# Performance work log

Measured on AMD Instinct MI355X. Metric: run time of the kernel, lower is better.

Reference implementation:

```python
import jax, jax.numpy as jnp
import numpy as np

N, F, E, T = 50000, 128, 800000, 8


def setup_inputs() -> dict:
    key = jax.random.key(0)
    ks = jax.random.split(key, 10)
    s = 1.0 / np.sqrt(F)
    return {
        "x": jax.random.normal(ks[0], (N, F), jnp.float32),
        "edge_index": jax.random.randint(ks[1], (2, E), 0, N, jnp.int64),
        "edge_weight": jax.random.uniform(ks[2], (E,), jnp.float32),
        "W0": jax.random.normal(ks[3], (F, F), jnp.float32) * s,
        "Wih": jax.random.normal(ks[4], (3 * F, F), jnp.float32) * s,
        "Whh": jax.random.normal(ks[5], (3 * F, F), jnp.float32) * s,
        "bih": jax.random.normal(ks[6], (3 * F,), jnp.float32) * s,
        "bhh": jax.random.normal(ks[7], (3 * F,), jnp.float32) * s,
        "Wlin": jax.random.normal(ks[8], (T, F), jnp.float32) * s,
        "blin": jax.random.normal(ks[9], (T,), jnp.float32) * s,
    }


def _evolve_weight(W0, Wih, Whh, bih, bhh):
    # One GRU step with input = hidden = W0 (rows of weight matrix as batch).
    gi = W0 @ Wih.T + bih  # [F, 3F]
    gh = W0 @ Whh.T + bhh
    ir, iz, inn = jnp.split(gi, 3, axis=1)
    hr, hz, hn = jnp.split(gh, 3, axis=1)
    r = jax.nn.sigmoid(ir + hr)
    z = jax.nn.sigmoid(iz + hz)
    n = jnp.tanh(inn + r * hn)
    return (1.0 - z) * n + z * W0  # [F, F]


def reference(x, edge_index, edge_weight, W0, Wih, Whh, bih, bhh, Wlin, blin):
    n_nodes = x.shape[0]
    W = _evolve_weight(W0, Wih, Whh, bih, bhh)
    # gcn_norm with added self-loops (fill value 1.0), symmetric normalization
    loop = jnp.arange(n_nodes, dtype=edge_index.dtype)
    row = jnp.concatenate([edge_index[0], loop])
    col = jnp.concatenate([edge_index[1], loop])
    ew = jnp.concatenate([edge_weight, jnp.ones((n_nodes,), edge_weight.dtype)])
    deg = jax.ops.segment_sum(ew, col, num_segments=n_nodes)
    dinv = jnp.where(deg > 0, jax.lax.rsqrt(jnp.where(deg > 0, deg, 1.0)), 0.0)
    norm = dinv[row] * ew * dinv[col]  # [E+N]
    xw = x @ W  # [N, F]
    h = jax.ops.segment_sum(norm[:, None] * xw[row], col, num_segments=n_nodes)
    h = jax.nn.relu(h)
    return h @ Wlin.T + blin  # [N, n_target]
```

## Files before the change

### kernel.cpp

```cpp
#include <hip/hip_runtime.h>
#include <math.h>

#define F 128
#define FIX_SCALE 16777216.0f
#define FIX_INV   (1.0f / 16777216.0f)
#define CNT_SHIFT 40
#define DEG_MASK  ((1ULL << 40) - 1)
#define EVB 256

using bf16x8 = __attribute__((ext_vector_type(8))) short;
using f32x4  = __attribute__((ext_vector_type(4))) float;

__device__ inline int read_idx(const int* ei, long long elem, int i64) {
    return i64 ? (int)((const long long*)ei)[elem] : ei[elem];
}
__device__ inline unsigned int f2bf_rn(float f) {
    unsigned int b = __float_as_uint(f);
    return (b + 0x7FFFu + ((b >> 16) & 1u)) >> 16;
}
__device__ inline float bflo(unsigned int u) { return __uint_as_float(u << 16); }
__device__ inline float bfhi(unsigned int u) { return __uint_as_float(u & 0xFFFF0000u); }

__device__ inline void acc8(float* acc, float wt, uint4 v) {
    acc[0] += wt * bflo(v.x); acc[1] += wt * bfhi(v.x);
    acc[2] += wt * bflo(v.y); acc[3] += wt * bfhi(v.y);
    acc[4] += wt * bflo(v.z); acc[5] += wt * bfhi(v.z);
    acc[6] += wt * bflo(v.w); acc[7] += wt * bfhi(v.w);
}

__global__ void k_init(unsigned long long* packed8, int* flag, const int* ei, int M8) {
    int i = blockIdx.x * blockDim.x + threadIdx.x;
    if (i < M8) packed8[i] = 0ULL;
    if (i == 0) {
        int i64 = 1;
        for (int j = 0; j < 32; ++j) if (ei[2 * j + 1] != 0) { i64 = 0; break; }
        *flag = i64;
    }
}

__global__ __launch_bounds__(256) void k_count_evolve(
        const int* __restrict__ ei, const float* __restrict__ ew,
        unsigned long long* __restrict__ packed8, int* __restrict__ pos,
        const int* __restrict__ flag, int E, int N,
        const float* __restrict__ W0, const float* __restrict__ Wih,
        const float* __restrict__ Whh, const float* __restrict__ bih,
        const float* __restrict__ bhh,
        unsigned short* __restrict__ Wth, unsigned short* __restrict__ Wtl) {
    int wave = threadIdx.x >> 6, lane = threadIdx.x & 63;
    if ((int)blockIdx.x >= EVB) {
        int e = ((int)blockIdx.x - EVB) * 256 + threadIdx.x;
        if (e >= E) return;
        int i64 = *flag;
        int c = read_idx(ei, (long long)E + e, i64);
        int copy = blockIdx.x & 7;
        unsigned long long u = (1ULL << CNT_SHIFT) |
                               (unsigned long long)(ew[e] * FIX_SCALE + 0.5f);
        unsigned long long old = atomicAdd(&packed8[(size_t)copy * N + c], u);
        pos[e] = (int)(((unsigned int)(old >> CNT_SHIFT)) | ((unsigned int)copy << 24));
        return;
    }
    int gw = (int)blockIdx.x * 4 + wave;
    int pairBase = gw * 16;
    int i = pairBase >> 7;
    int jb = pairBase & 127;
    int lp = lane & 15, sl = lane >> 4;
    int j = jb + lp;
    const float* w0p = W0 + (size_t)i * F;
    const float* pir = Wih + (size_t)j * F;
    const float* piz = Wih + (size_t)(j + F) * F;
    const float* pin = Wih + (size_t)(j + 2 * F) * F;
    const float* phr = Whh + (size_t)j * F;
    const float* phz = Whh + (size_t)(j + F) * F;
    const float* phn = Whh + (size_t)(j + 2 * F) * F;
    float air = 0, aiz = 0, ain = 0, ahr = 0, ahz = 0, ahn = 0;
    int k0 = sl * 32;
    #pragma unroll
    for (int kk = 0; kk < 32; kk += 4) {
        int k = k0 + kk;
        float4 w0 = *(const float4*)&w0p[k];
        float4 a;
        a = *(const float4*)&pir[k]; air += w0.x*a.x + w0.y*a.y + w0.z*a.z + w0.w*a.w;
        a = *(const float4*)&piz[k]; aiz += w0.x*a.x + w0.y*a.y + w0.z*a.z + w0.w*a.w;
        a = *(const float4*)&pin[k]; ain += w0.x*a.x + w0.y*a.y + w0.z*a.z + w0.w*a.w;
        a = *(const float4*)&phr[k]; ahr += w0.x*a.x + w0.y*a.y + w0.z*a.z + w0.w*a.w;
        a = *(const float4*)&phz[k]; ahz += w0.x*a.x + w0.y*a.y + w0.z*a.z + w0.w*a.w;
        a = *(const float4*)&phn[k]; ahn += w0.x*a.x + w0.y*a.y + w0.z*a.z + w0.w*a.w;
    }
    air += __shfl_xor(air, 16, 64); air += __shfl_xor(air, 32, 64);
    aiz += __shfl_xor(aiz, 16, 64); aiz += __shfl_xor(aiz, 32, 64);
    ain += __shfl_xor(ain, 16, 64); ain += __shfl_xor(ain, 32, 64);
    ahr += __shfl_xor(ahr, 16, 64); ahr += __shfl_xor(ahr, 32, 64);
    ahz += __shfl_xor(ahz, 16, 64); ahz += __shfl_xor(ahz, 32, 64);
    ahn += __shfl_xor(ahn, 16, 64); ahn += __shfl_xor(ahn, 32, 64);
    if (sl == 0) {
        air += bih[j];          ahr += bhh[j];
        aiz += bih[j + F];      ahz += bhh[j + F];
        ain += bih[j + 2 * F];  ahn += bhh[j + 2 * F];
        float r = 1.0f / (1.0f + expf(-(air + ahr)));
        float z = 1.0f / (1.0f + expf(-(aiz + ahz)));
        float n = tanhf(ain + r * ahn);
        float w = (1.0f - z) * n + z * w0p[j];
        unsigned int hb = f2bf_rn(w);
        float whi = __uint_as_float(hb << 16);
        unsigned int lb = f2bf_rn(w - whi);
        Wth[j * F + i] = (unsigned short)hb;
        Wtl[j * F + i] = (unsigned short)lb;
    }
}

__global__ void k_bsum(const unsigned long long* __restrict__ packed8,
                       int* __restrict__ bsum, int N) {
    __shared__ int s[4];
    int i = blockIdx.x * 256 + threadIdx.x;
    int v = 0;
    if (i < N) {
        #pragma unroll
        for (int k = 0; k < 8; ++k)
            v += (int)(packed8[(size_t)k * N + i] >> CNT_SHIFT);
    }
    #pragma unroll
    for (int o = 1; o < 64; o <<= 1) v += __shfl_xor(v, o, 64);
    if ((threadIdx.x & 63) == 0) s[threadIdx.x >> 6] = v;
    __syncthreads();
    if (threadIdx.x == 0) bsum[blockIdx.x] = s[0] + s[1] + s[2] + s[3];
}

__global__ void k_bscan(int* bsum, int nb) {
    __shared__ int sdata[1024];
    int tid = threadIdx.x;
    int run = 0;
    for (int base = 0; base < nb; base += 1024) {
        int i = base + tid;
        int v = (i < nb) ? bsum[i] : 0;
        sdata[tid] = v;
        __syncthreads();
        #pragma unroll
        for (int s = 1; s < 1024; s <<= 1) {
            int add = (tid >= s) ? sdata[tid - s] : 0;
            __syncthreads();
            sdata[tid] += add;
            __syncthreads();
        }
        if (i < nb) bsum[i] = run + sdata[tid] - v;
        run += sdata[1023];
        __syncthreads();
    }
}

__global__ void k_offs(const unsigned long long* __restrict__ packed8,
                       const int* __restrict__ bsum,
                       int* __restrict__ off, int* __restrict__ copyBase,
                       float* __restrict__ dinv, int N, int E) {
    __shared__ int sdata[256];
    int t = threadIdx.x;
    int i = blockIdx.x * 256 + t;
    int v = 0;
    unsigned long long dsum = 0;
    int cb[8];
    if (i < N) {
        int run = 0;
        #pragma unroll
        for (int k = 0; k < 8; ++k) {
            unsigned long long p = packed8[(size_t)k * N + i];
            cb[k] = run;
            run += (int)(p >> CNT_SHIFT);
            dsum += (p & DEG_MASK);
        }
        v = run;
        #pragma unroll
        for (int k = 0; k < 8; ++k) copyBase[(size_t)i * 8 + k] = cb[k];
    }
    sdata[t] = v;
    __syncthreads();
    #pragma unroll
    for (int s = 1; s < 256; s <<= 1) {
        int add = (t >= s) ? sdata[t - s] : 0;
        __syncthreads();
        sdata[t] += add;
        __syncthreads();
    }
    if (i < N) {
        off[i] = bsum[blockIdx.x] + sdata[t] - v;
        float deg = 1.0f + (float)dsum * FIX_INV;
        dinv[i] = rsqrtf(deg);
        if (i == N - 1) off[N] = E;
    }
}

__global__ __launch_bounds__(256) void k_place_cast(
        const int* __restrict__ ei, const float* __restrict__ ew,
        const int* __restrict__ off, const int* __restrict__ copyBase,
        const int* __restrict__ pos,
        int2* __restrict__ ep, const int* __restrict__ flag, int E, int placeBlocks,
        const float2* __restrict__ x2, const float* __restrict__ dinv,
        unsigned int* __restrict__ xs, int M) {
    if ((int)blockIdx.x < placeBlocks) {
        int e = blockIdx.x * 256 + threadIdx.x;
        if (e >= E) return;
        int i64 = *flag;
        int r = read_idx(ei, e, i64);
        int c = read_idx(ei, (long long)E + e, i64);
        int pe = pos[e];
        int slot = off[c] + copyBase[(size_t)c * 8 + (pe >> 24)] + (pe & 0xFFFFFF);
        ep[slot] = make_int2(r, __float_as_int(ew[e]));
    } else {
        int id = ((int)blockIdx.x - placeBlocks) * 256 + threadIdx.x;
        if (id >= M) return;
        float di = dinv[id >> 6];
        float2 v = x2[id];
        xs[id] = f2bf_rn(di * v.x) | (f2bf_rn(di * v.y) << 16);
    }
}

__global__ __launch_bounds__(256) void k_agg2(const uint4* __restrict__ xs4,
                                              const int* __restrict__ off,
                                              const int2* __restrict__ ep,
                                              const float* __restrict__ dinv,
                                              uint4* __restrict__ hagg4, int N) {
    int wave = threadIdx.x >> 6, lane = threadIdx.x & 63;
    int c = blockIdx.x * 4 + wave;
    if (c >= N) return;
    int g = lane >> 4, sl = lane & 15;
    int start = off[c], end = off[c + 1];
    float di = dinv[c];
    float a0[8] = {0,0,0,0,0,0,0,0}, a1[8] = {0,0,0,0,0,0,0,0};
    if (g == 0) {
        uint4 v = xs4[(size_t)c * 16 + sl];
        a0[0] = bflo(v.x); a0[1] = bfhi(v.x);
        a0[2] = bflo(v.y); a0[3] = bfhi(v.y);
        a0[4] = bflo(v.z); a0[5] = bfhi(v.z);
        a0[6] = bflo(v.w); a0[7] = bfhi(v.w);
    }
    int last = end - 1;
    for (int k = start; k < end; k += 16) {
        int iA = k + g, iB = k + g + 4, iC = k + g + 8, iD = k + g + 12;
        int2 eA = ep[min(iA, last)];
        int2 eB = ep[min(iB, last)];
        int2 eC = ep[min(iC, last)];
        int2 eD = ep[min(iD, last)];
        uint4 vA = xs4[(size_t)eA.x * 16 + sl];
        uint4 vB = xs4[(size_t)eB.x * 16 + sl];
        uint4 vC = xs4[(size_t)eC.x * 16 + sl];
        uint4 vD = xs4[(size_t)eD.x * 16 + sl];
        float wA = (iA <= last) ? __int_as_float(eA.y) : 0.f;
        float wB = (iB <= last) ? __int_as_float(eB.y) : 0.f;
        float wC = (iC <= last) ? __int_as_float(eC.y) : 0.f;
        float wD = (iD <= last) ? __int_as_float(eD.y) : 0.f;
        acc8(a0, wA, vA);
        acc8(a1, wB, vB);
        acc8(a0, wC, vC);
        acc8(a1, wD, vD);
    }
    #pragma unroll
    for (int f = 0; f < 8; ++f) {
        float v = a0[f] + a1[f];
        v += __shfl_xor(v, 16, 64);
        v += __shfl_xor(v, 32, 64);
        a0[f] = v;
    }
    if (lane < 16) {
        uint4 o;
        o.x = f2bf_rn(di * a0[0]) | (f2bf_rn(di * a0[1]) << 16);
        o.y = f2bf_rn(di * a0[2]) | (f2bf_rn(di * a0[3]) << 16);
        o.z = f2bf_rn(di * a0[4]) | (f2bf_rn(di * a0[5]) << 16);
        o.w = f2bf_rn(di * a0[6]) | (f2bf_rn(di * a0[7]) << 16);
        hagg4[(size_t)c * 16 + lane] = o;
    }
}

__global__ __launch_bounds__(256) void k_gemm(const uint4* __restrict__ hagg4,
                                              const unsigned short* __restrict__ Wth,
                                              const unsigned short* __restrict__ Wtl,
                                              const float* __restrict__ Wlin,
                                              const float* __restrict__ blin,
                                              float* __restrict__ out, int N) {
    __shared__ __align__(16) unsigned int At[64 * 68];
    __shared__ __align__(16) float WlinL[8 * F];
    int t = threadIdx.x;
    int row0 = blockIdx.x * 64;
    #pragma unroll
    for (int it = 0; it < 4; ++it) {
        int idx = it * 256 + t;
        int rr = idx >> 4, c4 = idx & 15;
        uint4 v = make_uint4(0u, 0u, 0u, 0u);
        if (row0 + rr < N) v = hagg4[(size_t)(row0 + rr) * 16 + c4];
        *(uint4*)&At[rr * 68 + c4 * 4] = v;
    }
    *(float4*)&WlinL[t * 4] = *(const float4*)&Wlin[t * 4];
    __syncthreads();

    int wave = t >> 6, lane = t & 63;
    int sl = lane & 15, q = lane >> 4;
    const unsigned short* Ash = (const unsigned short*)At;
    int mrow = wave * 16 + sl;

    f32x4 acc[8];
    #pragma unroll
    for (int nt = 0; nt < 8; ++nt) acc[nt] = (f32x4){0.f, 0.f, 0.f, 0.f};
    #pragma unroll
    for (int ko = 0; ko < 4; ++ko) {
        bf16x8 a = *(const bf16x8*)&Ash[mrow * 136 + ko * 32 + q * 8];
        #pragma unroll
        for (int nt = 0; nt < 8; ++nt) {
            int boff = (nt * 16 + sl) * F + ko * 32 + q * 8;
            bf16x8 bh = *(const bf16x8*)&Wth[boff];
            bf16x8 bl = *(const bf16x8*)&Wtl[boff];
            acc[nt] = __builtin_amdgcn_mfma_f32_16x16x32_bf16(a, bh, acc[nt], 0, 0, 0);
            acc[nt] = __builtin_amdgcn_mfma_f32_16x16x32_bf16(a, bl, acc[nt], 0, 0, 0);
        }
    }
    #pragma unroll
    for (int nt = 0; nt < 8; ++nt)
        #pragma unroll
        for (int r = 0; r < 4; ++r) acc[nt][r] = fmaxf(acc[nt][r], 0.f);

    float p[8][4];
    #pragma unroll
    for (int tt = 0; tt < 8; ++tt) {
        float wl[8];
        #pragma unroll
        for (int nt = 0; nt < 8; ++nt) wl[nt] = WlinL[tt * F + nt * 16 + sl];
        #pragma unroll
        for (int r = 0; r < 4; ++r) {
            float s = 0.f;
            #pragma unroll
            for (int nt = 0; nt < 8; ++nt) s += acc[nt][r] * wl[nt];
            p[tt][r] = s;
        }
    }
    #pragma unroll
    for (int tt = 0; tt < 8; ++tt)
        #pragma unroll
        for (int r = 0; r < 4; ++r) {
            float v = p[tt][r];
            v += __shfl_xor(v, 1, 64); v += __shfl_xor(v, 2, 64);
            v += __shfl_xor(v, 4, 64); v += __shfl_xor(v, 8, 64);
            p[tt][r] = v;
        }
    if (sl == 0) {
        #pragma unroll
        for (int r = 0; r < 4; ++r) {
            int row = row0 + wave * 16 + q * 4 + r;
            if (row < N) {
                #pragma unroll
                for (int tt = 0; tt < 8; ++tt)
                    out[(size_t)row * 8 + tt] = p[tt][r] + blin[tt];
            }
        }
    }
}

extern "C" void kernel_launch(void* const* d_in, const int* in_sizes, int n_in,
                              void* d_out, int out_size, void* d_ws, size_t ws_size,
                              hipStream_t stream) {
    const float* x    = (const float*)d_in[0];
    const int*   ei   = (const int*)d_in[1];
    const float* ew   = (const float*)d_in[2];
    const float* W0   = (const float*)d_in[3];
    const float* Wih  = (const float*)d_in[4];
    const float* Whh  = (const float*)d_in[5];
    const float* bih  = (const float*)d_in[6];
    const float* bhh  = (const float*)d_in[7];
    const float* Wlin = (const float*)d_in[8];
    const float* blin = (const float*)d_in[9];
    int N = in_sizes[0] / F;
    int E = in_sizes[1] / 2;
    float* outp = (float*)d_out;

    int nblk = (N + 255) / 256;
    int cntBlocks = (E + 255) / 256;
    int M = N * 64;
    int M8 = N * 8;

    char* wsb = (char*)d_ws;
    size_t cur = 0;
    auto alloc = [&](size_t sz) -> void* {
        void* p = wsb + cur;
        cur = (cur + sz + 255) & ~(size_t)255;
        return p;
    };
    unsigned long long* packed8 = (unsigned long long*)alloc((size_t)M8 * 8);
    float* dinv = (float*)alloc((size_t)N * 4);
    int*   off  = (int*)  alloc((size_t)(N + 1) * 4);
    int*   bsum = (int*)  alloc((size_t)nblk * 4);
    int*   flag = (int*)  alloc(256);
    int*   pos  = (int*)  alloc((size_t)E * 4);
    int*   copyBase = (int*)alloc((size_t)N * 8 * 4);
    int2*  ep   = (int2*) alloc((size_t)E * 8);
    unsigned short* Wth = (unsigned short*)alloc((size_t)F * F * 2);
    unsigned short* Wtl = (unsigned short*)alloc((size_t)F * F * 2);
    unsigned int* xs    = (unsigned int*)alloc((size_t)N * 64 * 4);
    unsigned int* hagg  = (unsigned int*)alloc((size_t)N * 64 * 4);
    (void)ws_size; (void)n_in; (void)out_size;

    hipLaunchKernelGGL(k_init, dim3((M8 + 255) / 256), dim3(256), 0, stream, packed8, flag, ei, M8);
    hipLaunchKernelGGL(k_count_evolve, dim3(EVB + cntBlocks), dim3(256), 0, stream,
                       ei, ew, packed8, pos, flag, E, N,
                       W0, Wih, Whh, bih, bhh, Wth, Wtl);
    hipLaunchKernelGGL(k_bsum,  dim3(nblk), dim3(256),  0, stream, packed8, bsum, N);
    hipLaunchKernelGGL(k_bscan, dim3(1),    dim3(1024), 0, stream, bsum, nblk);
    hipLaunchKernelGGL(k_offs,  dim3(nblk), dim3(256),  0, stream, packed8, bsum, off, copyBase, dinv, N, E);
    hipLaunchKernelGGL(k_place_cast, dim3(cntBlocks + (M + 255) / 256), dim3(256), 0, stream,
                       ei, ew, off, copyBase, pos, ep, flag, E, cntBlocks,
                       (const float2*)x, dinv, xs, M);
    hipLaunchKernelGGL(k_agg2, dim3((N + 3) / 4), dim3(256), 0, stream,
                       (const uint4*)xs, off, ep, dinv, (uint4*)hagg, N);
    hipLaunchKernelGGL(k_gemm, dim3((N + 63) / 64), dim3(256), 0, stream,
                       (const uint4*)hagg, Wth, Wtl, Wlin, blin, outp, N);
}
```

Measured before the change: 219.6 us.

## Fuse block-sum, scan and offset kernels into one cooperative grid-sync kernel

Replaces the three-kernel bsum/bscan/offs pipeline with a single cooperative kernel that computes per-block counts, does a grid sync, lets block 0 scan the block sums, and syncs again before writing offsets and dinv. It also drops the init kernel in favour of a memset and detects the int64 index format per block instead of through a global flag. The aim is to cut launch count and kernel-boundary overhead, at the cost of grid-sync latency and a serial scan inside a single block.

```diff
diff --git a/kernel.cpp b/kernel.cpp
--- a/kernel.cpp
+++ b/kernel.cpp
@@ -1,4 +1,5 @@
 #include <hip/hip_runtime.h>
+#include <hip/hip_cooperative_groups.h>
 #include <math.h>
 
 #define F 128
@@ -28,29 +29,30 @@
     acc[6] += wt * bflo(v.w); acc[7] += wt * bfhi(v.w);
 }
 
-__global__ void k_init(unsigned long long* packed8, int* flag, const int* ei, int M8) {
-    int i = blockIdx.x * blockDim.x + threadIdx.x;
-    if (i < M8) packed8[i] = 0ULL;
-    if (i == 0) {
+__device__ inline int detect_i64(const int* ei, int* sh) {
+    if (threadIdx.x == 0) {
         int i64 = 1;
         for (int j = 0; j < 32; ++j) if (ei[2 * j + 1] != 0) { i64 = 0; break; }
-        *flag = i64;
-    }
+        *sh = i64;
+    }
+    __syncthreads();
+    return *sh;
 }
 
 __global__ __launch_bounds__(256) void k_count_evolve(
         const int* __restrict__ ei, const float* __restrict__ ew,
         unsigned long long* __restrict__ packed8, int* __restrict__ pos,
-        const int* __restrict__ flag, int E, int N,
+        int E, int N,
         const float* __restrict__ W0, const float* __restrict__ Wih,
         const float* __restrict__ Whh, const float* __restrict__ bih,
         const float* __restrict__ bhh,
         unsigned short* __restrict__ Wth, unsigned short* __restrict__ Wtl) {
+    __shared__ int i64sh;
     int wave = threadIdx.x >> 6, lane = threadIdx.x & 63;
     if ((int)blockIdx.x >= EVB) {
+        int i64 = detect_i64(ei, &i64sh);
         int e = ((int)blockIdx.x - EVB) * 256 + threadIdx.x;
         if (e >= E) return;
-        int i64 = *flag;
         int c = read_idx(ei, (long long)E + e, i64);
         int copy = blockIdx.x & 7;
         unsigned long long u = (1ULL << CNT_SHIFT) |
@@ -108,57 +110,18 @@
     }
 }
 
-__global__ void k_bsum(const unsigned long long* __restrict__ packed8,
-                       int* __restrict__ bsum, int N) {
-    __shared__ int s[4];
-    int i = blockIdx.x * 256 + threadIdx.x;
-    int v = 0;
-    if (i < N) {
-        #pragma unroll
-        for (int k = 0; k < 8; ++k)
-            v += (int)(packed8[(size_t)k * N + i] >> CNT_SHIFT);
-    }
-    #pragma unroll
-    for (int o = 1; o < 64; o <<= 1) v += __shfl_xor(v, o, 64);
-    if ((threadIdx.x & 63) == 0) s[threadIdx.x >> 6] = v;
-    __syncthreads();
-    if (threadIdx.x == 0) bsum[blockIdx.x] = s[0] + s[1] + s[2] + s[3];
-}
-
-__global__ void k_bscan(int* bsum, int nb) {
-    __shared__ int sdata[1024];
-    int tid = threadIdx.x;
-    int run = 0;
-    for (int base = 0; base < nb; base += 1024) {
-        int i = base + tid;
-        int v = (i < nb) ? bsum[i] : 0;
-        sdata[tid] = v;
-        __syncthreads();
-        #pragma unroll
-        for (int s = 1; s < 1024; s <<= 1) {
-            int add = (tid >= s) ? sdata[tid - s] : 0;
-            __syncthreads();
-            sdata[tid] += add;
-            __syncthreads();
-        }
-        if (i < nb) bsum[i] = run + sdata[tid] - v;
-        run += sdata[1023];
-        __syncthreads();
-    }
-}
-
-__global__ void k_offs(const unsigned long long* __restrict__ packed8,
-                       const int* __restrict__ bsum,
-                       int* __restrict__ off, int* __restrict__ copyBase,
-                       float* __restrict__ dinv, int N, int E) {
+__global__ __launch_bounds__(256) void k_scan(const unsigned long long* __restrict__ packed8,
+        int* __restrict__ bsum, int* __restrict__ off, int* __restrict__ copyBase,
+        float* __restrict__ dinv, int N, int E, int nblk) {
+    cooperative_groups::grid_group grid = cooperative_groups::this_grid();
     __shared__ int sdata[256];
-    int t = threadIdx.x;
-    int i = blockIdx.x * 256 + t;
+    int t = threadIdx.x, b = blockIdx.x;
+    int i = b * 256 + t;
     int v = 0;
     unsigned long long dsum = 0;
-    int cb[8];
     if (i < N) {
         int run = 0;
+        int cb[8];
         #pragma unroll
         for (int k = 0; k < 8; ++k) {
             unsigned long long p = packed8[(size_t)k * N + i];
@@ -179,10 +142,35 @@
         sdata[t] += add;
         __syncthreads();
     }
+    int incl = sdata[t];
+    if (t == 255) bsum[b] = incl;
+    __threadfence();
+    grid.sync();
+    if (b == 0) {
+        int run = 0;
+        for (int base = 0; base < nblk; base += 256) {
+            int idx = base + t;
+            int bv = (idx < nblk) ? bsum[idx] : 0;
+            __syncthreads();
+            sdata[t] = bv;
+            __syncthreads();
+            #pragma unroll
+            for (int s = 1; s < 256; s <<= 1) {
+                int add = (t >= s) ? sdata[t - s] : 0;
+                __syncthreads();
+                sdata[t] += add;
+                __syncthreads();
+            }
+            if (idx < nblk) bsum[idx] = run + sdata[t] - bv;
+            run += sdata[255];
+            __syncthreads();
+        }
+        __threadfence();
+    }
+    grid.sync();
     if (i < N) {
-        off[i] = bsum[blockIdx.x] + sdata[t] - v;
-        float deg = 1.0f + (float)dsum * FIX_INV;
-        dinv[i] = rsqrtf(deg);
+        off[i] = bsum[b] + incl - v;
+        dinv[i] = rsqrtf(1.0f + (float)dsum * FIX_INV);
         if (i == N - 1) off[N] = E;
     }
 }
@@ -191,17 +179,18 @@
         const int* __restrict__ ei, const float* __restrict__ ew,
         const int* __restrict__ off, const int* __restrict__ copyBase,
         const int* __restrict__ pos,
-        int2* __restrict__ ep, const int* __restrict__ flag, int E, int placeBlocks,
+        int2* __restrict__ ep, int E, int placeBlocks,
         const float2* __restrict__ x2, const float* __restrict__ dinv,
         unsigned int* __restrict__ xs, int M) {
+    __shared__ int i64sh;
     if ((int)blockIdx.x < placeBlocks) {
+        int i64 = detect_i64(ei, &i64sh);
         int e = blockIdx.x * 256 + threadIdx.x;
         if (e >= E) return;
-        int i64 = *flag;
         int r = read_idx(ei, e, i64);
         int c = read_idx(ei, (long long)E + e, i64);
         int pe = pos[e];
-        int slot = off[c] + copyBase[(size_t)c * 8 + (pe >> 24)] + (pe & 0xFFFFFF);
+        int slot = off[c] + copyBase[(size_t)c * 8 + ((unsigned int)pe >> 24)] + (pe & 0xFFFFFF);
         ep[slot] = make_int2(r, __float_as_int(ew[e]));
     } else {
         int id = ((int)blockIdx.x - placeBlocks) * 256 + threadIdx.x;
@@ -383,7 +372,6 @@
     float* dinv = (float*)alloc((size_t)N * 4);
     int*   off  = (int*)  alloc((size_t)(N + 1) * 4);
     int*   bsum = (int*)  alloc((size_t)nblk * 4);
-    int*   flag = (int*)  alloc(256);
     int*   pos  = (int*)  alloc((size_t)E * 4);
     int*   copyBase = (int*)alloc((size_t)N * 8 * 4);
     int2*  ep   = (int2*) alloc((size_t)E * 8);
@@ -393,15 +381,17 @@
     unsigned int* hagg  = (unsigned int*)alloc((size_t)N * 64 * 4);
     (void)ws_size; (void)n_in; (void)out_size;
 
-    hipLaunchKernelGGL(k_init, dim3((M8 + 255) / 256), dim3(256), 0, stream, packed8, flag, ei, M8);
+    hipMemsetAsync(packed8, 0, (size_t)M8 * 8, stream);
     hipLaunchKernelGGL(k_count_evolve, dim3(EVB + cntBlocks), dim3(256), 0, stream,
-                       ei, ew, packed8, pos, flag, E, N,
+                       ei, ew, packed8, pos, E, N,
                        W0, Wih, Whh, bih, bhh, Wth, Wtl);
-    hipLaunchKernelGGL(k_bsum,  dim3(nblk), dim3(256),  0, stream, packed8, bsum, N);
-    hipLaunchKernelGGL(k_bscan, dim3(1),    dim3(1024), 0, stream, bsum, nblk);
-    hipLaunchKernelGGL(k_offs,  dim3(nblk), dim3(256),  0, stream, packed8, bsum, off, copyBase, dinv, N, E);
+    {
+        void* args[] = { (void*)&packed8, (void*)&bsum, (void*)&off, (void*)&copyBase,
+                         (void*)&dinv, (void*)&N, (void*)&E, (void*)&nblk };
+        hipLaunchCooperativeKernel((void*)k_scan, dim3(nblk), dim3(256), args, 0, stream);
+    }
     hipLaunchKernelGGL(k_place_cast, dim3(cntBlocks + (M + 255) / 256), dim3(256), 0, stream,
-                       ei, ew, off, copyBase, pos, ep, flag, E, cntBlocks,
+                       ei, ew, off, copyBase, pos, ep, E, cntBlocks,
                        (const float2*)x, dinv, xs, M);
     hipLaunchKernelGGL(k_agg2, dim3((N + 3) / 4), dim3(256), 0, stream,
                        (const uint4*)xs, off, ep, dinv, (uint4*)hagg, N);
```

New measurement: 292.5 us. 33.2% more time.
